# Optimization experiments

Measured on AMD Instinct MI355X. Metric: run time of the kernel, lower is better.

Reference implementation:

```python
import jax, jax.numpy as jnp
import numpy as np

B, S, H, NH, HD = 2, 1024, 1024, 16, 64
L, C, E, K, D = 256, 2048, 8, 2, 2048
EPS = 1e-5


def _ln(x):
    m = x.mean(-1, keepdims=True)
    v = x.var(-1, keepdims=True)
    return (x - m) * jax.lax.rsqrt(v + EPS)


def _rot_half(x):
    h = x.shape[-1] // 2
    return jnp.concatenate([-x[..., h:], x[..., :h]], axis=-1)


def _attn(q, k, v, scale):
    s = jnp.einsum('bhqd,bhkd->bhqk', q, k) * scale
    p = jax.nn.softmax(s, axis=-1)
    return jnp.einsum('bhqk,bhkd->bhqd', p, v)


def _forward(x, condition, enc, rope_cos, rope_sin, adaln_w, adaln_b, qw, qb, kw, kb, vw, vb, ow, ob, cqw, cqb, ckw, ckb, cvw, cvb, cow, cob, cn_g, cn_b, gate_w, ew1, eb1, ew2, eb2):
    b, s, hdim = x.shape
    # AdaLN-Zero modulation params (condition is per-sample vector)
    mod = jax.nn.silu(condition) @ adaln_w + adaln_b
    sh1, sc1, g1, sh2, sc2, g2 = jnp.split(mod, 6, axis=-1)
    # --- self-attention with RoPE ---
    h = _ln(x) * (1 + sc1[:, None]) + sh1[:, None]
    q = (h @ qw + qb).reshape(b, s, NH, HD).transpose(0, 2, 1, 3)
    k = (h @ kw + kb).reshape(b, s, NH, HD).transpose(0, 2, 1, 3)
    v = (h @ vw + vb).reshape(b, s, NH, HD).transpose(0, 2, 1, 3)
    cos = rope_cos[None, None]
    sin = rope_sin[None, None]
    q = q * cos + _rot_half(q) * sin
    k = k * cos + _rot_half(k) * sin
    a = _attn(q, k, v, 1.0 / np.sqrt(HD)).transpose(0, 2, 1, 3).reshape(b, s, hdim)
    x = x + g1[:, None] * (a @ ow + ob)
    # --- cross-attention (affine LayerNorm) ---
    hc = _ln(x) * cn_g + cn_b
    lq = (hc @ cqw + cqb).reshape(b, s, NH, HD).transpose(0, 2, 1, 3)
    lk = (enc @ ckw + ckb).reshape(b, -1, NH, HD).transpose(0, 2, 1, 3)
    lv = (enc @ cvw + cvb).reshape(b, -1, NH, HD).transpose(0, 2, 1, 3)
    ca = _attn(lq, lk, lv, 1.0 / np.sqrt(HD)).transpose(0, 2, 1, 3).reshape(b, s, hdim)
    x = x + ca @ cow + cob
    # --- MoE FFN with AdaLN-Zero modulation ---
    h = _ln(x) * (1 + sc2[:, None]) + sh2[:, None]
    logits = h @ gate_w                                   # [B,S,E]
    probs = jax.nn.softmax(logits, axis=-1)
    topp, topi = jax.lax.top_k(probs, K)                  # [B,S,K]
    topp = topp / topp.sum(-1, keepdims=True)
    onehot = jax.nn.one_hot(topi, E, dtype=x.dtype)       # [B,S,K,E]
    cw = (onehot * topp[..., None]).sum(-2)               # [B,S,E] combine weights
    tokens_per_expert = onehot.sum(-2).mean(0)            # [S,E] (matches torch one_hot(...).sum(-2).mean(0))
    avg_prob = probs.mean((0, 1))                         # [E]
    aux = E * (tokens_per_expert * avg_prob).sum()
    hf = h.reshape(-1, hdim)                              # [T,H]
    act = jax.nn.gelu(jnp.einsum('th,ehd->ted', hf, ew1) + eb1, approximate=False)
    y = jnp.einsum('ted,edh->teh', act, ew2) + eb2        # [T,E,H]
    moe = jnp.einsum('te,teh->th', cw.reshape(-1, E), y).reshape(b, s, hdim)
    x = x + g2[:, None] * moe
    return x, aux


def setup_inputs() -> dict:
    key = jax.random.key(0)
    ks = jax.random.split(key, 30)
    w = lambda i, shape: (jax.random.normal(ks[i], shape) * 0.02).astype(jnp.float32)
    pos = jnp.arange(S, dtype=jnp.float32)[:, None]
    inv = 1.0 / (10000.0 ** (jnp.arange(0, HD, 2, dtype=jnp.float32) / HD))
    ang = jnp.concatenate([pos * inv[None, :]] * 2, axis=-1)  # [S,HD]
    return dict(
        x=jax.random.normal(ks[0], (B, S, H), jnp.float32),
        condition=jax.random.normal(ks[1], (B, H), jnp.float32),
        enc=jax.random.normal(ks[2], (B, L, C), jnp.float32),
        rope_cos=jnp.cos(ang).astype(jnp.float32),
        rope_sin=jnp.sin(ang).astype(jnp.float32),
        adaln_w=w(3, (H, 6 * H)), adaln_b=w(4, (6 * H,)),
        qw=w(5, (H, H)), qb=w(6, (H,)), kw=w(7, (H, H)), kb=w(8, (H,)),
        vw=w(9, (H, H)), vb=w(10, (H,)), ow=w(11, (H, H)), ob=w(12, (H,)),
        cqw=w(13, (H, H)), cqb=w(14, (H,)), ckw=w(15, (C, H)), ckb=w(16, (H,)),
        cvw=w(17, (C, H)), cvb=w(18, (H,)), cow=w(19, (H, H)), cob=w(20, (H,)),
        cn_g=jnp.ones((H,), jnp.float32), cn_b=jnp.zeros((H,), jnp.float32),
        gate_w=w(21, (H, E)),
        ew1=w(22, (E, H, D)), eb1=w(23, (E, D)),
        ew2=w(24, (E, D, H)), eb2=w(25, (E, H)),
    )


def reference(x, condition, enc, rope_cos, rope_sin, adaln_w, adaln_b, qw, qb, kw, kb, vw, vb, ow, ob, cqw, cqb, ckw, ckb, cvw, cvb, cow, cob, cn_g, cn_b, gate_w, ew1, eb1, ew2, eb2):
    return _forward(x, condition, enc, rope_cos, rope_sin, adaln_w, adaln_b, qw, qb, kw, kb, vw, vb, ow, ob, cqw, cqb, ckw, ckb, cvw, cvb, cow, cob, cn_g, cn_b, gate_w, ew1, eb1, ew2, eb2)
```

## Files before the change

### kernel.cpp

```cpp
#include <hip/hip_runtime.h>
#include <math.h>

#define Hh 1024
#define Ss 1024
#define Bb 2
#define NHh 16
#define HDd 64
#define Tt 2048
#define Ll 256
#define Cc 2048
#define Ee 8
#define Dd 2048
#define EPSf 1e-5f
#define PADROWS 5120

using bf16x8 = __attribute__((ext_vector_type(8))) short;
using f32x4  = __attribute__((ext_vector_type(4))) float;
using ushort8 = __attribute__((ext_vector_type(8))) unsigned short;

__device__ __forceinline__ float geluf(float x) {
    return 0.5f * x * (1.0f + erff(x * 0.70710678118654752f));
}

__device__ __forceinline__ unsigned short f2bf(float x) {
    union { float f; unsigned int u; } c; c.f = x;
    unsigned int r = (c.u + 0x7fffu + ((c.u >> 16) & 1u)) >> 16;
    return (unsigned short)r;
}

__device__ __forceinline__ void gload16(const void* g, void* l) {
    __builtin_amdgcn_global_load_lds(
        (const __attribute__((address_space(1))) void*)g,
        (__attribute__((address_space(3))) void*)l, 16, 0, 0);
}

__device__ __forceinline__ void tcast_tile(const float* __restrict__ src,
        unsigned short* __restrict__ dst, int R, int C, int lt,
        unsigned short* __restrict__ tb, int tid) {
    int gx = R >> 7;
    int rt = lt % gx, ct = lt / gx;
    int r0 = rt * 128, c0 = ct * 64;
    int lr = tid >> 4;
    int lc4 = (tid & 15) << 2;
    #pragma unroll
    for (int p = 0; p < 8; ++p) {
        int row = lr + 16 * p;
        float4 v = *(const float4*)&src[(size_t)(r0 + row) * C + c0 + lc4];
        ushort4 h; h.x = f2bf(v.x); h.y = f2bf(v.y); h.z = f2bf(v.z); h.w = f2bf(v.w);
        *(ushort4*)&tb[row * 70 + lc4] = h;
    }
    __syncthreads();
    int wr = tid >> 5;
    int wc4 = (tid & 31) << 2;
    #pragma unroll
    for (int p = 0; p < 8; ++p) {
        int orow = wr + 8 * p;
        ushort4 o;
        o.x = tb[(wc4 + 0) * 70 + orow];
        o.y = tb[(wc4 + 1) * 70 + orow];
        o.z = tb[(wc4 + 2) * 70 + orow];
        o.w = tb[(wc4 + 3) * 70 + orow];
        *(ushort4*)&dst[(size_t)(c0 + orow) * R + r0 + wc4] = o;
    }
}

__device__ __forceinline__ void tcast_tile512(const float* __restrict__ src,
        unsigned short* __restrict__ dst, int R, int C, int lt,
        unsigned short* __restrict__ tb, int tid) {
    int gx = R >> 7;
    int rt = lt % gx, ct = lt / gx;
    int r0 = rt * 128, c0 = ct * 64;
    int lr = tid >> 4;
    int lc4 = (tid & 15) << 2;
    #pragma unroll
    for (int p = 0; p < 4; ++p) {
        int row = lr + 32 * p;
        float4 v = *(const float4*)&src[(size_t)(r0 + row) * C + c0 + lc4];
        ushort4 h; h.x = f2bf(v.x); h.y = f2bf(v.y); h.z = f2bf(v.z); h.w = f2bf(v.w);
        *(ushort4*)&tb[row * 70 + lc4] = h;
    }
    __syncthreads();
    int wr = tid >> 5;
    int wc4 = (tid & 31) << 2;
    #pragma unroll
    for (int p = 0; p < 4; ++p) {
        int orow = wr + 16 * p;
        ushort4 o;
        o.x = tb[(wc4 + 0) * 70 + orow];
        o.y = tb[(wc4 + 1) * 70 + orow];
        o.z = tb[(wc4 + 2) * 70 + orow];
        o.w = tb[(wc4 + 3) * 70 + orow];
        *(ushort4*)&dst[(size_t)(c0 + orow) * R + r0 + wc4] = o;
    }
}

__global__ __launch_bounds__(256) void prep_all(
        const float* __restrict__ qw, const float* __restrict__ kw, const float* __restrict__ vw,
        const float* __restrict__ qb, const float* __restrict__ kb, const float* __restrict__ vb,
        const float* __restrict__ ckb, const float* __restrict__ cvb,
        unsigned short* __restrict__ qkvwT, float* __restrict__ qkvb, float* __restrict__ ckvb) {
    __shared__ unsigned short tb[128 * 70];
    int bid = blockIdx.x;
    int tid = threadIdx.x;
    if (bid < 384) {
        int seg = bid >> 7;
        int lt = bid & 127;
        const float* src = (seg == 0) ? qw : (seg == 1 ? kw : vw);
        unsigned short* dst = qkvwT + (size_t)seg * 1024 * 1024;
        tcast_tile(src, dst, 1024, 1024, lt, tb, tid);
        return;
    }
    int i = (bid - 384) * 256 + tid;
    if (i < 1024) qkvb[i] = qb[i];
    else if (i < 2048) qkvb[i] = kb[i - 1024];
    else if (i < 3072) qkvb[i] = vb[i - 2048];
    else if (i < 4096) ckvb[i - 3072] = ckb[i - 3072];
    else if (i < 5120) ckvb[i - 3072] = cvb[i - 4096];
}

__global__ __launch_bounds__(256) void vtrans16(const unsigned short* __restrict__ in,
        unsigned short* __restrict__ out, int S) {
    __shared__ unsigned short sm[32][36];
    int bh = blockIdx.z;
    int s0 = blockIdx.x * 32, d0 = blockIdx.y * 32;
    int lr = threadIdx.x >> 3, lc = (threadIdx.x & 7) << 2;
    ushort4 v = *(const ushort4*)&in[((size_t)bh * S + s0 + lr) * 64 + d0 + lc];
    sm[lr][lc] = v.x; sm[lr][lc + 1] = v.y; sm[lr][lc + 2] = v.z; sm[lr][lc + 3] = v.w;
    __syncthreads();
    ushort4 o;
    o.x = sm[lc + 0][lr]; o.y = sm[lc + 1][lr]; o.z = sm[lc + 2][lr]; o.w = sm[lc + 3][lr];
    *(ushort4*)&out[((size_t)bh * 64 + d0 + lr) * S + s0 + lc] = o;
}

__global__ __launch_bounds__(256) void adaln_kernel(const float* __restrict__ cond,
        const float* __restrict__ w, const float* __restrict__ b, float* __restrict__ mod) {
    __shared__ float ss[Hh];
    int bi = (blockIdx.x * 256) / (6 * Hh);
    const float* cp = cond + (size_t)bi * Hh;
    for (int i = threadIdx.x; i < Hh; i += 256) {
        float c = cp[i];
        ss[i] = c / (1.0f + expf(-c));
    }
    __syncthreads();
    int idx = blockIdx.x * 256 + threadIdx.x;
    int j = idx % (6 * Hh);
    float acc = b[j];
    for (int i = 0; i < Hh; ++i) acc += ss[i] * w[(size_t)i * (6 * Hh) + j];
    mod[idx] = acc;
}

template<int OM>
__global__ __launch_bounds__(256) void ln_affine(const float* __restrict__ X, float* __restrict__ O32,
        unsigned short* __restrict__ O16,
        const float* __restrict__ scale, const float* __restrict__ shift, int bstride, float add1) {
    int t = blockIdx.x;
    int tid = threadIdx.x;
    const float* xr = X + (size_t)t * Hh;
    float4 xv = *(const float4*)&xr[tid * 4];
    float s = xv.x + xv.y + xv.z + xv.w;
    float q = xv.x * xv.x + xv.y * xv.y + xv.z * xv.z + xv.w * xv.w;
    #pragma unroll
    for (int off = 32; off > 0; off >>= 1) {
        s += __shfl_down(s, off);
        q += __shfl_down(q, off);
    }
    __shared__ float rsum[4], rsq[4];
    __shared__ float smean, srstd;
    int wv = tid >> 6, ln = tid & 63;
    if (ln == 0) { rsum[wv] = s; rsq[wv] = q; }
    __syncthreads();
    if (tid == 0) {
        float ts = rsum[0] + rsum[1] + rsum[2] + rsum[3];
        float tq = rsq[0] + rsq[1] + rsq[2] + rsq[3];
        float mean = ts * (1.0f / Hh);
        float var = tq * (1.0f / Hh) - mean * mean;
        smean = mean; srstd = rsqrtf(var + EPSf);
    }
    __syncthreads();
    float mean = smean, rstd = srstd;
    int bi = t >> 10;
    int j = tid * 4;
    const float* scp = scale + (size_t)bi * bstride;
    const float* shp = shift + (size_t)bi * bstride;
    float4 sc4 = *(const float4*)&scp[j];
    float4 sh4 = *(const float4*)&shp[j];
    float4 o;
    o.x = (xv.x - mean) * rstd * (add1 + sc4.x) + sh4.x;
    o.y = (xv.y - mean) * rstd * (add1 + sc4.y) + sh4.y;
    o.z = (xv.z - mean) * rstd * (add1 + sc4.z) + sh4.z;
    o.w = (xv.w - mean) * rstd * (add1 + sc4.w) + sh4.w;
    if (OM & 1) *(float4*)&O32[(size_t)t * Hh + j] = o;
    if (OM & 2) {
        ushort4 h; h.x = f2bf(o.x); h.y = f2bf(o.y); h.z = f2bf(o.z); h.w = f2bf(o.w);
        *(ushort4*)&O16[(size_t)t * Hh + j] = h;
    }
}

__global__ __launch_bounds__(512) void gemm_qkv(const unsigned short* __restrict__ A,
        const unsigned short* __restrict__ Bt, const float* __restrict__ bias,
        unsigned short* __restrict__ P0, unsigned short* __restrict__ P1,
        unsigned short* __restrict__ P2, const float* __restrict__ rc, const float* __restrict__ rsn,
        const float* __restrict__ ow, const float* __restrict__ cqw, const float* __restrict__ cow,
        const float* __restrict__ ckw, const float* __restrict__ cvw, const float* __restrict__ enc,
        unsigned short* __restrict__ owT, unsigned short* __restrict__ cqwT,
        unsigned short* __restrict__ cowT, unsigned short* __restrict__ ckvwT,
        unsigned short* __restrict__ encb, int K) {
    __shared__ unsigned short sh[2 * 128 * 32 * 2];
    int tid = threadIdx.x;
    if (blockIdx.y >= 24) {
        int t = blockIdx.x + 16 * (blockIdx.y - 24);
        if (t < 384) {
            int seg = t >> 7, lt = t & 127;
            const float* src = (seg == 0) ? ow : (seg == 1 ? cqw : cow);
            unsigned short* dst = (seg == 0) ? owT : (seg == 1 ? cqwT : cowT);
            tcast_tile512(src, dst, 1024, 1024, lt, sh, tid);
        } else if (t < 896) {
            int t2 = t - 384;
            const float* src = (t2 < 256) ? ckw : cvw;
            unsigned short* dst = (t2 < 256) ? ckvwT : (ckvwT + (size_t)1024 * 2048);
            tcast_tile512(src, dst, 2048, 1024, t2 & 255, sh, tid);
        } else {
            int i = (t - 896) * 512 + tid;
            float4 v = ((const float4*)enc)[i];
            ushort4 o; o.x = f2bf(v.x); o.y = f2bf(v.y); o.z = f2bf(v.z); o.w = f2bf(v.w);
            ((ushort4*)encb)[i] = o;
        }
        return;
    }
    unsigned short* As0 = sh;
    unsigned short* Bs0 = sh + 2 * 128 * 32;
    int m0 = blockIdx.x * 128, n0 = blockIdx.y * 128;
    int lane = tid & 63;
    int wv = tid >> 6;
    int wm = (wv >> 1) * 32, wn = (wv & 1) * 64;
    f32x4 acc[2][4] = {};
    int r0 = tid >> 2, q8 = (tid & 3) * 8;
    const unsigned short* gA = A + (size_t)(m0 + r0) * K + q8;
    const unsigned short* gB = Bt + (size_t)(n0 + r0) * K + q8;
    int ra = (lane & 15) * 32 + (lane >> 4) * 8;
    auto stage = [&](int kk, int bufi) {
        gload16(gA + kk, &As0[bufi * 128 * 32 + tid * 8]);
        gload16(gB + kk, &Bs0[bufi * 128 * 32 + tid * 8]);
    };
    int nsteps = K / 32;
    stage(0, 0);
    int cur = 0;
    for (int s = 0; s < nsteps; ++s) {
        if (s + 1 < nsteps) {
            stage((s + 1) * 32, cur ^ 1);
            asm volatile("s_waitcnt vmcnt(2)" ::: "memory");
        } else {
            asm volatile("s_waitcnt vmcnt(0)" ::: "memory");
        }
        __builtin_amdgcn_s_barrier();
        bf16x8 af[2], bf[4];
        #pragma unroll
        for (int f = 0; f < 2; ++f) af[f] = *(const bf16x8*)&As0[cur * 128 * 32 + (wm + f * 16) * 32 + ra];
        #pragma unroll
        for (int f = 0; f < 4; ++f) bf[f] = *(const bf16x8*)&Bs0[cur * 128 * 32 + (wn + f * 16) * 32 + ra];
        #pragma unroll
        for (int i = 0; i < 2; ++i)
            #pragma unroll
            for (int j = 0; j < 4; ++j)
                acc[i][j] = __builtin_amdgcn_mfma_f32_16x16x32_bf16(af[i], bf[j], acc[i][j], 0, 0, 0);
        asm volatile("s_waitcnt lgkmcnt(0)" ::: "memory");
        __builtin_amdgcn_s_barrier();
        cur ^= 1;
    }
    int colb = n0 + wn + (lane & 15);
    int rowb = m0 + wm + (lane >> 4) * 4;
    float bv[4];
    #pragma unroll
    for (int j = 0; j < 4; ++j) bv[j] = bias[colb + j * 16];
    int nh = (colb >> 6) & 15;
    int type = colb >> 10;
    float qs = (type == 0) ? 0.125f : 1.0f;
    #pragma unroll
    for (int i = 0; i < 2; ++i) {
        #pragma unroll
        for (int r = 0; r < 4; ++r) {
            int row = rowb + i * 16 + r;
            int b = row >> 10, s = row & 1023;
            unsigned short* dst = (type == 0) ? P0 : (type == 1 ? P1 : P2);
            size_t obase = ((size_t)((b * 16 + nh) * 1024 + s)) * 64;
            if (type < 2) {
                #pragma unroll
                for (int j = 0; j < 2; ++j) {
                    int hd = j * 16 + (lane & 15);
                    float v0 = acc[i][j][r] + bv[j];
                    float v2 = acc[i][j + 2][r] + bv[j + 2];
                    float c1 = rc[s * 64 + hd], s1 = rsn[s * 64 + hd];
                    float c2 = rc[s * 64 + hd + 32], s2 = rsn[s * 64 + hd + 32];
                    dst[obase + hd] = f2bf((v0 * c1 - v2 * s1) * qs);
                    dst[obase + hd + 32] = f2bf((v2 * c2 + v0 * s2) * qs);
                }
            } else {
                #pragma unroll
                for (int j = 0; j < 4; ++j)
                    dst[obase + j * 16 + (lane & 15)] = f2bf(acc[i][j][r] + bv[j]);
            }
        }
    }
}

template<int EP>
__global__ __launch_bounds__(256) void gemm64(const unsigned short* __restrict__ A,
        const unsigned short* __restrict__ Bt, const float* __restrict__ bias,
        float* __restrict__ Cf, unsigned short* __restrict__ P0, unsigned short* __restrict__ P1,
        const float* __restrict__ baseb, const float* __restrict__ gatep,
        int M, int N, int K) {
    __shared__ unsigned short As[2][64 * 32];
    __shared__ unsigned short Bs[2][64 * 32];
    int m0 = blockIdx.x * 64, n0 = blockIdx.y * 64;
    int tid = threadIdx.x;
    int lane = tid & 63;
    int wv = tid >> 6;
    int wm = (wv >> 1) * 32, wn = (wv & 1) * 32;
    f32x4 acc[2][2] = {};
    int r0 = tid >> 2, q8 = (tid & 3) * 8;
    const unsigned short* gA = A + (size_t)(m0 + r0) * K + q8;
    const unsigned short* gB = Bt + (size_t)(n0 + r0) * K + q8;
    int ra = (lane & 15) * 32 + (lane >> 4) * 8;
    auto stage = [&](int kk, int bufi) {
        gload16(gA + kk, &As[bufi][tid * 8]);
        gload16(gB + kk, &Bs[bufi][tid * 8]);
    };
    int nsteps = K / 32;
    stage(0, 0);
    int cur = 0;
    for (int s = 0; s < nsteps; ++s) {
        if (s + 1 < nsteps) {
            stage((s + 1) * 32, cur ^ 1);
            asm volatile("s_waitcnt vmcnt(2)" ::: "memory");
        } else {
            asm volatile("s_waitcnt vmcnt(0)" ::: "memory");
        }
        __builtin_amdgcn_s_barrier();
        bf16x8 af[2], bf[2];
        #pragma unroll
        for (int f = 0; f < 2; ++f) {
            af[f] = *(const bf16x8*)&As[cur][(wm + f * 16) * 32 + ra];
            bf[f] = *(const bf16x8*)&Bs[cur][(wn + f * 16) * 32 + ra];
        }
        #pragma unroll
        for (int i = 0; i < 2; ++i)
            #pragma unroll
            for (int j = 0; j < 2; ++j)
                acc[i][j] = __builtin_amdgcn_mfma_f32_16x16x32_bf16(af[i], bf[j], acc[i][j], 0, 0, 0);
        asm volatile("s_waitcnt lgkmcnt(0)" ::: "memory");
        __builtin_amdgcn_s_barrier();
        cur ^= 1;
    }
    int colb = n0 + wn + (lane & 15);
    int rowb = m0 + wm + (lane >> 4) * 4;
    float bv[2];
    #pragma unroll
    for (int j = 0; j < 2; ++j) bv[j] = bias[colb + j * 16];
    if (EP == 0 || EP == 4 || EP == 5) {
        #pragma unroll
        for (int j = 0; j < 2; ++j) {
            int col = colb + j * 16;
            #pragma unroll
            for (int i = 0; i < 2; ++i)
                #pragma unroll
                for (int r = 0; r < 4; ++r) {
                    int row = rowb + i * 16 + r;
                    size_t gi = (size_t)row * N + col;
                    float v = acc[i][j][r] + bv[j];
                    if (EP == 0) {
                        Cf[gi] = v;
                    } else if (EP == 4) {
                        float g = gatep[(row >> 10) * (6 * Hh) + col];
                        Cf[gi] = baseb[gi] + g * v;
                    } else {
                        Cf[gi] = baseb[gi] + v;
                    }
                }
        }
        return;
    }
    int nh = (colb >> 6) & 15;
    int type = colb >> 10;
    int hd0 = colb & 63;
    #pragma unroll
    for (int i = 0; i < 2; ++i) {
        #pragma unroll
        for (int r = 0; r < 4; ++r) {
            int row = rowb + i * 16 + r;
            if (EP == 2) {
                int b = row >> 8, s = row & 255;
                unsigned short* dst = (type == 0) ? P0 : P1;
                size_t obase = ((size_t)((b * 16 + nh) * 256 + s)) * 64;
                #pragma unroll
                for (int j = 0; j < 2; ++j)
                    dst[obase + hd0 + j * 16] = f2bf(acc[i][j][r] + bv[j]);
            } else {
                int b = row >> 10, s = row & 1023;
                size_t obase = ((size_t)((b * 16 + nh) * 1024 + s)) * 64;
                #pragma unroll
                for (int j = 0; j < 2; ++j)
                    P0[obase + hd0 + j * 16] = f2bf((acc[i][j][r] + bv[j]) * 0.125f);
            }
        }
    }
}

__global__ __launch_bounds__(512) void gemm_moe1(const unsigned short* __restrict__ A,
        const unsigned short* __restrict__ W, const float* __restrict__ bias,
        unsigned short* __restrict__ Og, const int* __restrict__ cnt,
        const int* __restrict__ offp, const int* __restrict__ gtok) {
    __shared__ unsigned short As[2][128 * 32];
    __shared__ unsigned short Bs[2][128 * 32];
    int m0 = blockIdx.x * 128;
    if (m0 >= offp[Ee]) return;
    int e = 0;
    while (offp[e + 1] <= m0) ++e;
    int base = offp[e], valid = cnt[e];
    int n0 = blockIdx.y * 128;
    int tid = threadIdx.x;
    int lane = tid & 63;
    int wv = tid >> 6;
    int wm = (wv >> 1) * 32, wn = (wv & 1) * 64;
    f32x4 acc[2][4] = {};
    int r0 = tid >> 2, q8 = (tid & 3) * 8;
    int lr0 = m0 - base + r0;
    int tok0 = gtok[base + (lr0 < valid ? lr0 : 0)];
    const unsigned short* gA = A + (size_t)tok0 * Hh + q8;
    const unsigned short* Wt = W + (size_t)e * Dd * Hh;
    const unsigned short* gB = Wt + (size_t)(n0 + r0) * Hh + q8;
    int ra = (lane & 15) * 32 + (lane >> 4) * 8;
    auto stage = [&](int kk, int bufi) {
        gload16(gA + kk, &As[bufi][tid * 8]);
        gload16(gB + kk, &Bs[bufi][tid * 8]);
    };
    int nsteps = Hh / 32;
    stage(0, 0);
    int cur = 0;
    for (int s = 0; s < nsteps; ++s) {
        if (s + 1 < nsteps) {
            stage((s + 1) * 32, cur ^ 1);
            asm volatile("s_waitcnt vmcnt(2)" ::: "memory");
        } else {
            asm volatile("s_waitcnt vmcnt(0)" ::: "memory");
        }
        __builtin_amdgcn_s_barrier();
        bf16x8 af[2], bf[4];
        #pragma unroll
        for (int f = 0; f < 2; ++f) af[f] = *(const bf16x8*)&As[cur][(wm + f * 16) * 32 + ra];
        #pragma unroll
        for (int f = 0; f < 4; ++f) bf[f] = *(const bf16x8*)&Bs[cur][(wn + f * 16) * 32 + ra];
        #pragma unroll
        for (int i = 0; i < 2; ++i)
            #pragma unroll
            for (int j = 0; j < 4; ++j)
                acc[i][j] = __builtin_amdgcn_mfma_f32_16x16x32_bf16(af[i], bf[j], acc[i][j], 0, 0, 0);
        asm volatile("s_waitcnt lgkmcnt(0)" ::: "memory");
        __builtin_amdgcn_s_barrier();
        cur ^= 1;
    }
    int colb = n0 + wn + (lane & 15);
    int rowtb = wm + (lane >> 4) * 4;
    const float* bp = bias + (size_t)e * Dd;
    #pragma unroll
    for (int j = 0; j < 4; ++j) {
        int col = colb + j * 16;
        float bv = bp[col];
        #pragma unroll
        for (int i = 0; i < 2; ++i) {
            #pragma unroll
            for (int r = 0; r < 4; ++r) {
                int rt = rowtb + i * 16 + r;
                if (m0 - base + rt < valid)
                    Og[(size_t)(m0 + rt) * Dd + col] = f2bf(geluf(acc[i][j][r] + bv));
            }
        }
    }
}

__global__ __launch_bounds__(512) void gemm_moe2(const unsigned short* __restrict__ A,
        const unsigned short* __restrict__ W, const float* __restrict__ bias,
        float* __restrict__ y, const int* __restrict__ cnt,
        const int* __restrict__ offp) {
    __shared__ unsigned short As[2][128 * 32];
    __shared__ unsigned short Bs[2][128 * 32];
    int m0 = blockIdx.x * 128;
    if (m0 >= offp[Ee]) return;
    int e = 0;
    while (offp[e + 1] <= m0) ++e;
    int base = offp[e], valid = cnt[e];
    int n0 = blockIdx.y * 128;
    int kz = blockIdx.z;
    int k0 = kz * (Dd / 2);
    int tid = threadIdx.x;
    int lane = tid & 63;
    int wv = tid >> 6;
    int wm = (wv >> 1) * 32, wn = (wv & 1) * 64;
    f32x4 acc[2][4] = {};
    int r0 = tid >> 2, q8 = (tid & 3) * 8;
    const unsigned short* gA = A + (size_t)(m0 + r0) * Dd + k0 + q8;
    const unsigned short* Wt = W + (size_t)e * Hh * Dd;
    const unsigned short* gB = Wt + (size_t)(n0 + r0) * Dd + k0 + q8;
    int ra = (lane & 15) * 32 + (lane >> 4) * 8;
    auto stage = [&](int kk, int bufi) {
        gload16(gA + kk, &As[bufi][tid * 8]);
        gload16(gB + kk, &Bs[bufi][tid * 8]);
    };
    int nsteps = (Dd / 2) / 32;
    stage(0, 0);
    int cur = 0;
    for (int s = 0; s < nsteps; ++s) {
        if (s + 1 < nsteps) {
            stage((s + 1) * 32, cur ^ 1);
            asm volatile("s_waitcnt vmcnt(2)" ::: "memory");
        } else {
            asm volatile("s_waitcnt vmcnt(0)" ::: "memory");
        }
        __builtin_amdgcn_s_barrier();
        bf16x8 af[2], bf[4];
        #pragma unroll
        for (int f = 0; f < 2; ++f) af[f] = *(const bf16x8*)&As[cur][(wm + f * 16) * 32 + ra];
        #pragma unroll
        for (int f = 0; f < 4; ++f) bf[f] = *(const bf16x8*)&Bs[cur][(wn + f * 16) * 32 + ra];
        #pragma unroll
        for (int i = 0; i < 2; ++i)
            #pragma unroll
            for (int j = 0; j < 4; ++j)
                acc[i][j] = __builtin_amdgcn_mfma_f32_16x16x32_bf16(af[i], bf[j], acc[i][j], 0, 0, 0);
        asm volatile("s_waitcnt lgkmcnt(0)" ::: "memory");
        __builtin_amdgcn_s_barrier();
        cur ^= 1;
    }
    int colb = n0 + wn + (lane & 15);
    int rowtb = wm + (lane >> 4) * 4;
    const float* bp = bias + (size_t)e * Hh;
    float* yz = y + (size_t)kz * PADROWS * Hh;
    #pragma unroll
    for (int j = 0; j < 4; ++j) {
        int col = colb + j * 16;
        float bv = (kz == 0) ? bp[col] : 0.0f;
        #pragma unroll
        for (int i = 0; i < 2; ++i) {
            #pragma unroll
            for (int r = 0; r < 4; ++r) {
                int rt = rowtb + i * 16 + r;
                int g = m0 + rt;
                if (g - base < valid)
                    yz[(size_t)g * Hh + col] = acc[i][j][r] + bv;
            }
        }
    }
}

__global__ __launch_bounds__(256) void moe_combine(const float* __restrict__ y,
        const int* __restrict__ gpos, const float* __restrict__ gwt,
        const float* __restrict__ gate2, float* __restrict__ outp) {
    int t = blockIdx.x;
    int j = threadIdx.x * 4;
    int g0 = gpos[2 * t], g1 = gpos[2 * t + 1];
    float w0 = gwt[g0], w1 = gwt[g1];
    const float* g2p = gate2 + (size_t)(t >> 10) * (6 * Hh);
    const size_t soff = (size_t)PADROWS * Hh;
    float4 a0 = *(const float4*)&y[(size_t)g0 * Hh + j];
    float4 a1 = *(const float4*)&y[soff + (size_t)g0 * Hh + j];
    float4 b0 = *(const float4*)&y[(size_t)g1 * Hh + j];
    float4 b1 = *(const float4*)&y[soff + (size_t)g1 * Hh + j];
    float4 g2 = *(const float4*)&g2p[j];
    float4 o = *(const float4*)&outp[(size_t)t * Hh + j];
    o.x += g2.x * (w0 * (a0.x + a1.x) + w1 * (b0.x + b1.x));
    o.y += g2.y * (w0 * (a0.y + a1.y) + w1 * (b0.y + b1.y));
    o.z += g2.z * (w0 * (a0.z + a1.z) + w1 * (b0.z + b1.z));
    o.w += g2.w * (w0 * (a0.w + a1.w) + w1 * (b0.w + b1.w));
    *(float4*)&outp[(size_t)t * Hh + j] = o;
}

__global__ __launch_bounds__(256) void fattn_m(const unsigned short* __restrict__ Qp,
        const unsigned short* __restrict__ Kp, const unsigned short* __restrict__ Vtp,
        unsigned short* __restrict__ O, int Skv,
        const float* __restrict__ ew1, const float* __restrict__ ew2,
        unsigned short* __restrict__ ew1T, unsigned short* __restrict__ ew2T) {
    __shared__ unsigned short shbuf[4 * 64 * 72];
    int tid = threadIdx.x;
    if (blockIdx.y >= 32) {
        int tile = blockIdx.x + 16 * (blockIdx.y - 32);
        if (tile < 2048) {
            int e = tile >> 8, lt = tile & 255;
            tcast_tile(ew1 + (size_t)e * 1024 * 2048, ew1T + (size_t)e * 2048 * 1024,
                       1024, 2048, lt, shbuf, tid);
        } else {
            int t2 = tile - 2048;
            int e = t2 >> 8, lt = t2 & 255;
            tcast_tile(ew2 + (size_t)e * 2048 * 1024, ew2T + (size_t)e * 1024 * 2048,
                       2048, 1024, lt, shbuf, tid);
        }
        return;
    }
    unsigned short* Qs  = shbuf;
    unsigned short* Ks  = shbuf + 64 * 72;
    unsigned short* Vts = shbuf + 2 * 64 * 72;
    unsigned short* Ps  = shbuf + 3 * 64 * 72;
    int q0 = blockIdx.x * 64;
    int bh = blockIdx.y;
    int b = bh >> 4, nh = bh & 15;
    int lane = tid & 63, w = tid >> 6;
    int sr = tid >> 2, sp = (tid & 3) * 16;
    {
        const unsigned short* src = &Qp[((size_t)bh * 1024 + q0 + sr) * 64 + sp];
        *(ushort8*)&Qs[sr * 72 + sp] = *(const ushort8*)&src[0];
        *(ushort8*)&Qs[sr * 72 + sp + 8] = *(const ushort8*)&src[8];
    }
    f32x4 acc[4] = {};
    float m_old[4], l_run[4];
    #pragma unroll
    for (int r = 0; r < 4; ++r) { m_old[r] = -1e30f; l_run[r] = 0.0f; }
    int wrow = w * 16;
    int k8 = (lane >> 4) * 8;
    ushort8 pkA, pkB, pvA, pvB;
    {
        const unsigned short* ksrc = &Kp[((size_t)bh * Skv + sr) * 64 + sp];
        pkA = *(const ushort8*)&ksrc[0];
        pkB = *(const ushort8*)&ksrc[8];
        const unsigned short* vsrc = &Vtp[((size_t)bh * 64 + sr) * Skv + sp];
        pvA = *(const ushort8*)&vsrc[0];
        pvB = *(const ushort8*)&vsrc[8];
    }
    for (int k0 = 0; k0 < Skv; k0 += 64) {
        asm volatile("s_waitcnt lgkmcnt(0)" ::: "memory");
        __builtin_amdgcn_s_barrier();
        *(ushort8*)&Ks[sr * 72 + sp] = pkA;
        *(ushort8*)&Ks[sr * 72 + sp + 8] = pkB;
        *(ushort8*)&Vts[sr * 72 + sp] = pvA;
        *(ushort8*)&Vts[sr * 72 + sp + 8] = pvB;
        if (k0 + 64 < Skv) {
            const unsigned short* ksrc = &Kp[((size_t)bh * Skv + k0 + 64 + sr) * 64 + sp];
            pkA = *(const ushort8*)&ksrc[0];
            pkB = *(const ushort8*)&ksrc[8];
            const unsigned short* vsrc = &Vtp[((size_t)bh * 64 + sr) * Skv + k0 + 64 + sp];
            pvA = *(const ushort8*)&vsrc[0];
            pvB = *(const ushort8*)&vsrc[8];
        }
        asm volatile("s_waitcnt lgkmcnt(0)" ::: "memory");
        __builtin_amdgcn_s_barrier();
        bf16x8 aq0 = *(const bf16x8*)&Qs[(wrow + (lane & 15)) * 72 + k8];
        bf16x8 aq1 = *(const bf16x8*)&Qs[(wrow + (lane & 15)) * 72 + 32 + k8];
        f32x4 sf[4];
        __builtin_amdgcn_s_setprio(1);
        #pragma unroll
        for (int j = 0; j < 4; ++j) {
            bf16x8 bk0 = *(const bf16x8*)&Ks[(j * 16 + (lane & 15)) * 72 + k8];
            bf16x8 bk1 = *(const bf16x8*)&Ks[(j * 16 + (lane & 15)) * 72 + 32 + k8];
            f32x4 z = {};
            z = __builtin_amdgcn_mfma_f32_16x16x32_bf16(aq0, bk0, z, 0, 0, 0);
            z = __builtin_amdgcn_mfma_f32_16x16x32_bf16(aq1, bk1, z, 0, 0, 0);
            sf[j] = z;
        }
        __builtin_amdgcn_s_setprio(0);
        float p[4][4];
        float fsc[4];
        #pragma unroll
        for (int r = 0; r < 4; ++r) {
            float mx = fmaxf(fmaxf(sf[0][r], sf[1][r]), fmaxf(sf[2][r], sf[3][r]));
            #pragma unroll
            for (int mk = 1; mk < 16; mk <<= 1) mx = fmaxf(mx, __shfl_xor(mx, mk));
            float mn = fmaxf(m_old[r], mx);
            float f = __expf(m_old[r] - mn);
            float rs = 0.0f;
            #pragma unroll
            for (int j = 0; j < 4; ++j) {
                p[j][r] = __expf(sf[j][r] - mn);
                rs += p[j][r];
            }
            #pragma unroll
            for (int mk = 1; mk < 16; mk <<= 1) rs += __shfl_xor(rs, mk);
            l_run[r] = l_run[r] * f + rs;
            m_old[r] = mn;
            fsc[r] = f;
        }
        #pragma unroll
        for (int jd = 0; jd < 4; ++jd)
            #pragma unroll
            for (int r = 0; r < 4; ++r) acc[jd][r] *= fsc[r];
        #pragma unroll
        for (int j = 0; j < 4; ++j)
            #pragma unroll
            for (int r = 0; r < 4; ++r)
                Ps[(wrow + (lane >> 4) * 4 + r) * 72 + j * 16 + (lane & 15)] = f2bf(p[j][r]);
        asm volatile("s_waitcnt lgkmcnt(0)" ::: "memory");
        __builtin_amdgcn_s_barrier();
        bf16x8 ap0 = *(const bf16x8*)&Ps[(wrow + (lane & 15)) * 72 + k8];
        bf16x8 ap1 = *(const bf16x8*)&Ps[(wrow + (lane & 15)) * 72 + 32 + k8];
        __builtin_amdgcn_s_setprio(1);
        #pragma unroll
        for (int jd = 0; jd < 4; ++jd) {
            bf16x8 bv0 = *(const bf16x8*)&Vts[(jd * 16 + (lane & 15)) * 72 + k8];
            bf16x8 bv1 = *(const bf16x8*)&Vts[(jd * 16 + (lane & 15)) * 72 + 32 + k8];
            acc[jd] = __builtin_amdgcn_mfma_f32_16x16x32_bf16(ap0, bv0, acc[jd], 0, 0, 0);
            acc[jd] = __builtin_amdgcn_mfma_f32_16x16x32_bf16(ap1, bv1, acc[jd], 0, 0, 0);
        }
        __builtin_amdgcn_s_setprio(0);
    }
    float inv[4];
    #pragma unroll
    for (int r = 0; r < 4; ++r) inv[r] = 1.0f / l_run[r];
    #pragma unroll
    for (int jd = 0; jd < 4; ++jd)
        #pragma unroll
        for (int r = 0; r < 4; ++r)
            O[((size_t)(b * Ss + q0 + wrow + (lane >> 4) * 4 + r)) * Hh + nh * 64 + jd * 16 + (lane & 15)]
                = f2bf(acc[jd][r] * inv[r]);
}

__global__ __launch_bounds__(256) void gate_kernel(const float* __restrict__ h,
        const float* __restrict__ gw, float* __restrict__ probs, int* __restrict__ topi,
        float* __restrict__ topw) {
    int t = blockIdx.x * 4 + (threadIdx.x >> 6);
    int lane = threadIdx.x & 63;
    const float* hp = h + (size_t)t * Hh;
    float lg[Ee] = {};
    #pragma unroll
    for (int s = 0; s < 4; ++s) {
        int d0 = s * 256 + lane * 4;
        float4 hv = *(const float4*)&hp[d0];
        float hv4[4] = {hv.x, hv.y, hv.z, hv.w};
        #pragma unroll
        for (int c = 0; c < 4; ++c) {
            float hx = hv4[c];
            const float* g0 = &gw[(size_t)(d0 + c) * Ee];
            #pragma unroll
            for (int e = 0; e < Ee; ++e) lg[e] += hx * g0[e];
        }
    }
    #pragma unroll
    for (int e = 0; e < Ee; ++e)
        #pragma unroll
        for (int mk = 1; mk < 64; mk <<= 1) lg[e] += __shfl_xor(lg[e], mk);
    if (lane == 0) {
        float m = lg[0];
        #pragma unroll
        for (int e = 1; e < Ee; ++e) m = fmaxf(m, lg[e]);
        float ssum = 0;
        #pragma unroll
        for (int e = 0; e < Ee; ++e) { lg[e] = expf(lg[e] - m); ssum += lg[e]; }
        float inv = 1.0f / ssum;
        #pragma unroll
        for (int e = 0; e < Ee; ++e) { lg[e] *= inv; probs[t * Ee + e] = lg[e]; }
        int i0 = 0;
        #pragma unroll
        for (int e = 1; e < Ee; ++e) if (lg[e] > lg[i0]) i0 = e;
        int i1 = (i0 == 0) ? 1 : 0;
        #pragma unroll
        for (int e = 0; e < Ee; ++e) if (e != i1 && e != i0 && lg[e] > lg[i1]) i1 = e;
        float w0 = lg[i0], w1 = lg[i1];
        float inv2 = 1.0f / (w0 + w1);
        topi[t * 2] = i0; topi[t * 2 + 1] = i1;
        topw[t * 2] = w0 * inv2; topw[t * 2 + 1] = w1 * inv2;
    }
}

__global__ __launch_bounds__(1024) void moe_prep(const float* __restrict__ probs,
        const int* __restrict__ topi, const float* __restrict__ topw,
        int* __restrict__ cnt, int* __restrict__ offp,
        int* __restrict__ gtok, float* __restrict__ gwt, int* __restrict__ gpos,
        float* __restrict__ auxout) {
    __shared__ int scnt[Ee], spos[Ee], soff[Ee + 1];
    __shared__ float sS[Ee], sC[Ee];
    int tid = threadIdx.x;
    if (tid < Ee) { scnt[tid] = 0; spos[tid] = 0; sS[tid] = 0.0f; sC[tid] = 0.0f; }
    __syncthreads();
    float lp[Ee] = {};
    float lc[Ee] = {};
    for (int t = tid; t < Tt; t += 1024) {
        int a0 = topi[2 * t], a1 = topi[2 * t + 1];
        atomicAdd(&scnt[a0], 1);
        atomicAdd(&scnt[a1], 1);
        #pragma unroll
        for (int e = 0; e < Ee; ++e) lp[e] += probs[t * Ee + e];
        lc[a0] += 1.0f; lc[a1] += 1.0f;
    }
    #pragma unroll
    for (int e = 0; e < Ee; ++e) {
        atomicAdd(&sS[e], lp[e]);
        atomicAdd(&sC[e], lc[e]);
    }
    __syncthreads();
    if (tid == 0) {
        int acc = 0;
        for (int e = 0; e < Ee; ++e) { soff[e] = acc; acc += (scnt[e] + 127) & ~127; }
        soff[Ee] = acc;
        float aux = 0.0f;
        for (int e = 0; e < Ee; ++e) aux += sS[e] * sC[e];
        auxout[0] = aux * (8.0f / 4096.0f);
    }
    if (tid < Ee) cnt[tid] = scnt[tid];
    __syncthreads();
    if (tid <= Ee) offp[tid] = soff[tid];
    for (int t = tid; t < Tt; t += 1024) {
        #pragma unroll
        for (int s = 0; s < 2; ++s) {
            int e = topi[2 * t + s];
            int pos = atomicAdd(&spos[e], 1);
            int g = soff[e] + pos;
            gtok[g] = t;
            gwt[g] = topw[2 * t + s];
            gpos[2 * t + s] = g;
        }
    }
}

extern "C" void kernel_launch(void* const* d_in, const int* in_sizes, int n_in,
                              void* d_out, int out_size, void* d_ws, size_t ws_size,
                              hipStream_t stream) {
    (void)in_sizes; (void)n_in; (void)out_size; (void)ws_size;
    const float* x    = (const float*)d_in[0];
    const float* cond = (const float*)d_in[1];
    const float* enc  = (const float*)d_in[2];
    const float* rc   = (const float*)d_in[3];
    const float* rsn  = (const float*)d_in[4];
    const float* adw  = (const float*)d_in[5];
    const float* adb  = (const float*)d_in[6];
    const float* qw  = (const float*)d_in[7];  const float* qb  = (const float*)d_in[8];
    const float* kw  = (const float*)d_in[9];  const float* kb2 = (const float*)d_in[10];
    const float* vw  = (const float*)d_in[11]; const float* vb  = (const float*)d_in[12];
    const float* ow  = (const float*)d_in[13]; const float* ob  = (const float*)d_in[14];
    const float* cqw = (const float*)d_in[15]; const float* cqb = (const float*)d_in[16];
    const float* ckw = (const float*)d_in[17]; const float* ckb = (const float*)d_in[18];
    const float* cvw = (const float*)d_in[19]; const float* cvb = (const float*)d_in[20];
    const float* cow = (const float*)d_in[21]; const float* cob = (const float*)d_in[22];
    const float* cng = (const float*)d_in[23]; const float* cnb = (const float*)d_in[24];
    const float* gatew = (const float*)d_in[25];
    const float* ew1 = (const float*)d_in[26]; const float* eb1 = (const float*)d_in[27];
    const float* ew2 = (const float*)d_in[28]; const float* eb2 = (const float*)d_in[29];
    float* out = (float*)d_out;

    char* ws = (char*)d_ws;
    size_t off = 0;
    auto alloc = [&](size_t bytes) {
        char* p = ws + off;
        off += (bytes + 255) & ~(size_t)255;
        return (void*)p;
    };
    float* hbuf   = (float*)alloc((size_t)Tt * Hh * 4);
    float* mod    = (float*)alloc((size_t)Bb * 6 * Hh * 4);
    float* probs  = (float*)alloc((size_t)Tt * Ee * 4);
    float* topw   = (float*)alloc((size_t)Tt * 2 * 4);
    int*   topi   = (int*)alloc((size_t)Tt * 2 * 4);
    float* qkvb   = (float*)alloc(3072 * 4);
    float* ckvb   = (float*)alloc(2048 * 4);
    int*   cntbuf = (int*)alloc(16 * 4);
    int*   offp   = (int*)alloc(16 * 4);
    int*   gtok   = (int*)alloc((size_t)PADROWS * 4);
    float* gwt    = (float*)alloc((size_t)PADROWS * 4);
    int*   gpos   = (int*)alloc((size_t)Tt * 2 * 4);
    typedef unsigned short u16;
    u16* h1b   = (u16*)alloc((size_t)Tt * Hh * 2);
    u16* hcb   = (u16*)alloc((size_t)Tt * Hh * 2);
    u16* h2b   = (u16*)alloc((size_t)Tt * Hh * 2);
    u16* abb   = (u16*)alloc((size_t)Tt * Hh * 2);
    u16* encb  = (u16*)alloc((size_t)Bb * Ll * Cc * 2);
    u16* actg  = (u16*)alloc((size_t)PADROWS * Dd * 2);
    u16* Qb16  = (u16*)alloc((size_t)32 * 1024 * 64 * 2);
    u16* Kb16  = (u16*)alloc((size_t)32 * 1024 * 64 * 2);
    u16* Vb16  = (u16*)alloc((size_t)32 * 1024 * 64 * 2);
    u16* Vt16  = (u16*)alloc((size_t)32 * 64 * 1024 * 2);
    u16* cQ16  = (u16*)alloc((size_t)32 * 1024 * 64 * 2);
    u16* cK16  = (u16*)alloc((size_t)32 * 256 * 64 * 2);
    u16* cV16  = (u16*)alloc((size_t)32 * 256 * 64 * 2);
    u16* cVt16 = (u16*)alloc((size_t)32 * 64 * 256 * 2);
    u16* qkvwT = (u16*)alloc((size_t)3072 * 1024 * 2);
    u16* owT   = (u16*)alloc((size_t)1024 * 1024 * 2);
    u16* cqwT  = (u16*)alloc((size_t)1024 * 1024 * 2);
    u16* ckvwT = (u16*)alloc((size_t)2048 * 2048 * 2);
    u16* cowT  = (u16*)alloc((size_t)1024 * 1024 * 2);
    u16* ew1T  = (u16*)alloc((size_t)Ee * Hh * Dd * 2);
    u16* ew2T  = (u16*)alloc((size_t)Ee * Dd * Hh * 2);
    float* ybuf = (float*)Qb16;

    dim3 blk(256);
    dim3 blk512(512);
    prep_all<<<dim3(404), blk, 0, stream>>>(qw, kw, vw, qb, kb2, vb, ckb, cvb,
        qkvwT, qkvb, ckvb);
    adaln_kernel<<<dim3(Bb * 6 * Hh / 256), blk, 0, stream>>>(cond, adw, adb, mod);
    ln_affine<2><<<dim3(Tt), blk, 0, stream>>>(x, nullptr, h1b, mod + Hh, mod + 0, 6 * Hh, 1.0f);
    gemm_qkv<<<dim3(16, 24 + 88), blk512, 0, stream>>>(h1b, qkvwT, qkvb,
        Qb16, Kb16, Vb16, rc, rsn,
        ow, cqw, cow, ckw, cvw, enc, owT, cqwT, cowT, ckvwT, encb, 1024);
    vtrans16<<<dim3(32, 2, 32), blk, 0, stream>>>(Vb16, Vt16, 1024);
    fattn_m<<<dim3(16, 32 + 256), blk, 0, stream>>>(Qb16, Kb16, Vt16, abb, 1024,
        ew1, ew2, ew1T, ew2T);
    gemm64<4><<<dim3(Tt / 64, Hh / 64), blk, 0, stream>>>(abb, owT, ob, out,
        nullptr, nullptr, x, mod + 2 * Hh, Tt, Hh, 1024);
    ln_affine<2><<<dim3(Tt), blk, 0, stream>>>(out, nullptr, hcb, cng, cnb, 0, 0.0f);
    gemm64<3><<<dim3(Tt / 64, Hh / 64), blk, 0, stream>>>(hcb, cqwT, cqb, nullptr,
        cQ16, nullptr, nullptr, nullptr, Tt, Hh, 1024);
    gemm64<2><<<dim3(Bb * Ll / 64, 2048 / 64), blk, 0, stream>>>(encb, ckvwT, ckvb, nullptr,
        cK16, cV16, nullptr, nullptr, Bb * Ll, 2048, Cc);
    vtrans16<<<dim3(8, 2, 32), blk, 0, stream>>>(cV16, cVt16, 256);
    fattn_m<<<dim3(16, 32), blk, 0, stream>>>(cQ16, cK16, cVt16, abb, 256,
        ew1, ew2, ew1T, ew2T);
    gemm64<5><<<dim3(Tt / 64, Hh / 64), blk, 0, stream>>>(abb, cowT, cob, out,
        nullptr, nullptr, out, nullptr, Tt, Hh, 1024);
    ln_affine<3><<<dim3(Tt), blk, 0, stream>>>(out, hbuf, h2b, mod + 4 * Hh, mod + 3 * Hh, 6 * Hh, 1.0f);
    gate_kernel<<<dim3(Tt / 4), blk, 0, stream>>>(hbuf, gatew, probs, topi, topw);
    moe_prep<<<dim3(1), dim3(1024), 0, stream>>>(probs, topi, topw, cntbuf, offp, gtok, gwt,
        gpos, out + (size_t)Tt * Hh);
    gemm_moe1<<<dim3(PADROWS / 128, Dd / 128), blk512, 0, stream>>>(h2b, ew1T, eb1, actg, cntbuf, offp, gtok);
    gemm_moe2<<<dim3(PADROWS / 128, Hh / 128, 2), blk512, 0, stream>>>(actg, ew2T, eb2, ybuf, cntbuf, offp);
    moe_combine<<<dim3(Tt), blk, 0, stream>>>(ybuf, gpos, gwt, mod + 5 * Hh, out);
}
```

Before: 390.9 us.

## Spread expert weight transpose-cast tiles across self-attention and projection GEMM launches

Expert weight fp32-to-bf16 transpose work, previously packed entirely into the self-attention launch as extra blocks, is split into four quarters. One quarter stays in the attention launch and the other three ride as extra blocks appended to three gemm64 launches. This is meant to balance the side work across kernels that otherwise underfill the GPU (gemm64 launches only 512 blocks), so the tail of the attention kernel shrinks. The gemm64 shared memory is merged into one larger buffer so the transpose tiles fit, which may reduce occupancy for the GEMM blocks.

```diff
diff --git a/kernel.cpp b/kernel.cpp
--- a/kernel.cpp
+++ b/kernel.cpp
@@ -13,6 +13,7 @@
 #define Dd 2048
 #define EPSf 1e-5f
 #define PADROWS 5120
+#define ESZ ((size_t)1024 * 2048)
 
 using bf16x8 = __attribute__((ext_vector_type(8))) short;
 using f32x4  = __attribute__((ext_vector_type(4))) float;
@@ -308,11 +309,17 @@
         const unsigned short* __restrict__ Bt, const float* __restrict__ bias,
         float* __restrict__ Cf, unsigned short* __restrict__ P0, unsigned short* __restrict__ P1,
         const float* __restrict__ baseb, const float* __restrict__ gatep,
-        int M, int N, int K) {
-    __shared__ unsigned short As[2][64 * 32];
-    __shared__ unsigned short Bs[2][64 * 32];
+        int M, int N, int K,
+        const float* __restrict__ pw, unsigned short* __restrict__ pwT, int pR, int pC) {
+    __shared__ unsigned short sh[8960];
+    int tid = threadIdx.x;
+    if (pw != nullptr && (int)blockIdx.y * 64 >= N) {
+        int t = blockIdx.x + gridDim.x * (blockIdx.y - (unsigned)(N / 64));
+        int e = t >> 8, lt = t & 255;
+        tcast_tile(pw + (size_t)e * ESZ, pwT + (size_t)e * ESZ, pR, pC, lt, sh, tid);
+        return;
+    }
     int m0 = blockIdx.x * 64, n0 = blockIdx.y * 64;
-    int tid = threadIdx.x;
     int lane = tid & 63;
     int wv = tid >> 6;
     int wm = (wv >> 1) * 32, wn = (wv & 1) * 32;
@@ -322,8 +329,8 @@
     const unsigned short* gB = Bt + (size_t)(n0 + r0) * K + q8;
     int ra = (lane & 15) * 32 + (lane >> 4) * 8;
     auto stage = [&](int kk, int bufi) {
-        gload16(gA + kk, &As[bufi][tid * 8]);
-        gload16(gB + kk, &Bs[bufi][tid * 8]);
+        gload16(gA + kk, &sh[bufi * 2048 + tid * 8]);
+        gload16(gB + kk, &sh[4096 + bufi * 2048 + tid * 8]);
     };
     int nsteps = K / 32;
     stage(0, 0);
@@ -339,8 +346,8 @@
         bf16x8 af[2], bf[2];
         #pragma unroll
         for (int f = 0; f < 2; ++f) {
-            af[f] = *(const bf16x8*)&As[cur][(wm + f * 16) * 32 + ra];
-            bf[f] = *(const bf16x8*)&Bs[cur][(wn + f * 16) * 32 + ra];
+            af[f] = *(const bf16x8*)&sh[cur * 2048 + (wm + f * 16) * 32 + ra];
+            bf[f] = *(const bf16x8*)&sh[4096 + cur * 2048 + (wn + f * 16) * 32 + ra];
         }
         #pragma unroll
         for (int i = 0; i < 2; ++i)
@@ -576,22 +583,13 @@
 __global__ __launch_bounds__(256) void fattn_m(const unsigned short* __restrict__ Qp,
         const unsigned short* __restrict__ Kp, const unsigned short* __restrict__ Vtp,
         unsigned short* __restrict__ O, int Skv,
-        const float* __restrict__ ew1, const float* __restrict__ ew2,
-        unsigned short* __restrict__ ew1T, unsigned short* __restrict__ ew2T) {
+        const float* __restrict__ ew1, unsigned short* __restrict__ ew1T) {
     __shared__ unsigned short shbuf[4 * 64 * 72];
     int tid = threadIdx.x;
     if (blockIdx.y >= 32) {
         int tile = blockIdx.x + 16 * (blockIdx.y - 32);
-        if (tile < 2048) {
-            int e = tile >> 8, lt = tile & 255;
-            tcast_tile(ew1 + (size_t)e * 1024 * 2048, ew1T + (size_t)e * 2048 * 1024,
-                       1024, 2048, lt, shbuf, tid);
-        } else {
-            int t2 = tile - 2048;
-            int e = t2 >> 8, lt = t2 & 255;
-            tcast_tile(ew2 + (size_t)e * 2048 * 1024, ew2T + (size_t)e * 1024 * 2048,
-                       2048, 1024, lt, shbuf, tid);
-        }
+        int e = tile >> 8, lt = tile & 255;
+        tcast_tile(ew1 + (size_t)e * ESZ, ew1T + (size_t)e * ESZ, 1024, 2048, lt, shbuf, tid);
         return;
     }
     unsigned short* Qs  = shbuf;
@@ -884,20 +882,24 @@
         Qb16, Kb16, Vb16, rc, rsn,
         ow, cqw, cow, ckw, cvw, enc, owT, cqwT, cowT, ckvwT, encb, 1024);
     vtrans16<<<dim3(32, 2, 32), blk, 0, stream>>>(Vb16, Vt16, 1024);
-    fattn_m<<<dim3(16, 32 + 256), blk, 0, stream>>>(Qb16, Kb16, Vt16, abb, 1024,
-        ew1, ew2, ew1T, ew2T);
-    gemm64<4><<<dim3(Tt / 64, Hh / 64), blk, 0, stream>>>(abb, owT, ob, out,
-        nullptr, nullptr, x, mod + 2 * Hh, Tt, Hh, 1024);
+    fattn_m<<<dim3(16, 32 + 64), blk, 0, stream>>>(Qb16, Kb16, Vt16, abb, 1024,
+        ew1, ew1T);
+    gemm64<4><<<dim3(Tt / 64, Hh / 64 + 32), blk, 0, stream>>>(abb, owT, ob, out,
+        nullptr, nullptr, x, mod + 2 * Hh, Tt, Hh, 1024,
+        ew1 + 4 * ESZ, ew1T + 4 * ESZ, 1024, 2048);
     ln_affine<2><<<dim3(Tt), blk, 0, stream>>>(out, nullptr, hcb, cng, cnb, 0, 0.0f);
-    gemm64<3><<<dim3(Tt / 64, Hh / 64), blk, 0, stream>>>(hcb, cqwT, cqb, nullptr,
-        cQ16, nullptr, nullptr, nullptr, Tt, Hh, 1024);
+    gemm64<3><<<dim3(Tt / 64, Hh / 64 + 32), blk, 0, stream>>>(hcb, cqwT, cqb, nullptr,
+        cQ16, nullptr, nullptr, nullptr, Tt, Hh, 1024,
+        ew2, ew2T, 2048, 1024);
     gemm64<2><<<dim3(Bb * Ll / 64, 2048 / 64), blk, 0, stream>>>(encb, ckvwT, ckvb, nullptr,
-        cK16, cV16, nullptr, nullptr, Bb * Ll, 2048, Cc);
+        cK16, cV16, nullptr, nullptr, Bb * Ll, 2048, Cc,
+        nullptr, nullptr, 0, 0);
     vtrans16<<<dim3(8, 2, 32), blk, 0, stream>>>(cV16, cVt16, 256);
     fattn_m<<<dim3(16, 32), blk, 0, stream>>>(cQ16, cK16, cVt16, abb, 256,
-        ew1, ew2, ew1T, ew2T);
-    gemm64<5><<<dim3(Tt / 64, Hh / 64), blk, 0, stream>>>(abb, cowT, cob, out,
-        nullptr, nullptr, out, nullptr, Tt, Hh, 1024);
+        ew1, ew1T);
+    gemm64<5><<<dim3(Tt / 64, Hh / 64 + 32), blk, 0, stream>>>(abb, cowT, cob, out,
+        nullptr, nullptr, out, nullptr, Tt, Hh, 1024,
+        ew2 + 4 * ESZ, ew2T + 4 * ESZ, 2048, 1024);
     ln_affine<3><<<dim3(Tt), blk, 0, stream>>>(out, hbuf, h2b, mod + 4 * Hh, mod + 3 * Hh, 6 * Hh, 1.0f);
     gate_kernel<<<dim3(Tt / 4), blk, 0, stream>>>(hbuf, gatew, probs, topi, topw);
     moe_prep<<<dim3(1), dim3(1024), 0, stream>>>(probs, topi, topw, cntbuf, offp, gtok, gwt,
```

Result: no change. 388.8 us (-0.5%).
